# Performance work log

Measured on AMD Instinct MI355X. Metric: run time of the kernel, lower is better.

The kernel has to match this reference:

```python
import jax, jax.numpy as jnp
import numpy as np

NPG = 400          # nodes per graph (CC400 atlas ROIs)
B = 512            # graphs per batch
N = B * NPG        # total nodes
EPG = 6400         # edges per graph (avg degree 16)
E = B * EPG
F_IN = 200         # node feature dim
H = 64             # hidden_channels
C = 2              # num_classes


def _lin(k, fi, fo):
    return jax.random.normal(k, (fi, fo), jnp.float32) / np.sqrt(fi)


def setup_inputs() -> dict:
    key = jax.random.key(0)
    ks = jax.random.split(key, 16)
    # intra-graph edges: local src/dst in [0, NPG) plus per-graph offset
    g = jnp.repeat(jnp.arange(B, dtype=jnp.int32), EPG)
    src = jax.random.randint(ks[0], (E,), 0, NPG, dtype=jnp.int32) + g * NPG
    dst = jax.random.randint(ks[1], (E,), 0, NPG, dtype=jnp.int32) + g * NPG
    edge_index = jnp.stack([src, dst])  # [2, E]
    x = jax.random.normal(ks[2], (N, F_IN), jnp.float32)
    return dict(
        x=x, edge_index=edge_index, npg=NPG,
        # SAGEConv i: out = lin_l(mean_agg) + lin_r(x); lin_l carries the bias
        W1l=_lin(ks[3], F_IN, H), W1r=_lin(ks[4], F_IN, H), b1=jnp.zeros((H,), jnp.float32),
        W2l=_lin(ks[5], H, H), W2r=_lin(ks[6], H, H), b2=jnp.zeros((H,), jnp.float32),
        W3l=_lin(ks[7], H, H), W3r=_lin(ks[8], H, H), b3=jnp.zeros((H,), jnp.float32),
        # SAGPooling score GNN = GraphConv(H, 1): lin_rel(sum_agg) + lin_root(x)
        Wpr=_lin(ks[9], H, 1), bpr=jnp.zeros((1,), jnp.float32), Wpo=_lin(ks[10], H, 1),
        # final classifier
        Wlin=_lin(ks[11], H, C), blin=jnp.zeros((C,), jnp.float32),
    )


def reference(x, edge_index, npg, W1l, W1r, b1, W2l, W2r, b2, W3l, W3r, b3,
              Wpr, bpr, Wpo, Wlin, blin):
    n = x.shape[0]
    src, dst = edge_index[0], edge_index[1]

    deg = jax.ops.segment_sum(jnp.ones((src.shape[0],), x.dtype), dst, num_segments=n)
    inv_deg = 1.0 / jnp.maximum(deg, 1.0)  # [n]

    def sage(h, Wl, Wr, b):
        # mean aggregation over incoming edges, then lin_l(agg)+b + lin_r(h)
        agg = jax.ops.segment_sum(h[src], dst, num_segments=n) * inv_deg[:, None]
        return agg @ Wl + b + h @ Wr

    x1 = jax.nn.relu(sage(x, W1l, W1r, b1))
    x2 = jax.nn.relu(sage(x1, W2l, W2r, b2)) + x1
    x3 = jax.nn.relu(sage(x2, W3l, W3r, b3)) + x2

    # SAGPooling score via GraphConv (add aggregation)
    score = (jax.ops.segment_sum(x3[src], dst, num_segments=n) @ Wpr + bpr
             + x3 @ Wpo)[:, 0]  # [n]

    nb = n // npg            # number of graphs
    k = npg // 2             # ratio = 0.5, uniform graph sizes
    vals, idx = jax.lax.top_k(score.reshape(nb, npg), k)       # [nb, k]
    flat_idx = (jnp.arange(nb, dtype=idx.dtype)[:, None] * npg + idx).reshape(-1)
    xp = x3[flat_idx] * jnp.tanh(vals.reshape(-1))[:, None]    # [nb*k, H]

    pooled = xp.reshape(nb, k, -1).mean(axis=1)                # global_mean_pool
    logits = pooled @ Wlin + blin
    return jax.nn.log_softmax(logits, axis=1)
```

## Files before the change

kernel.cpp:

```cpp
#include <hip/hip_runtime.h>
#include <hip/hip_bf16.h>
#include <math.h>

#define F_IN 200
#define HDIM 64
#define NPG  400
#define EPG  6400
#define KSEL 200

typedef __attribute__((ext_vector_type(4))) float f32x4;
typedef __attribute__((ext_vector_type(8))) short s16x8;
typedef __attribute__((ext_vector_type(4))) unsigned short u16x4;
typedef __attribute__((ext_vector_type(8))) unsigned short u16x8;

__device__ __forceinline__ void gload_lds16(const void* g, void* l) {
    __builtin_amdgcn_global_load_lds(
        (const __attribute__((address_space(1))) void*)g,
        (__attribute__((address_space(3))) void*)l, 16, 0, 0);
}

__device__ __forceinline__ unsigned int bf16_rne(float x) {
    unsigned int b = __float_as_uint(x);
    return (b + 0x7FFFu + ((b >> 16) & 1u)) >> 16;
}
__device__ __forceinline__ float frombf(unsigned short u) {
    return __uint_as_float(((unsigned int)u) << 16);
}

__device__ __forceinline__ void split8(f32x4 v0, f32x4 v1, s16x8& h, s16x8& l) {
    float x[8] = {v0.x, v0.y, v0.z, v0.w, v1.x, v1.y, v1.z, v1.w};
#pragma unroll
    for (int j = 0; j < 8; j++) {
        unsigned int hb = bf16_rne(x[j]);
        float hf = __uint_as_float(hb << 16);
        float r = x[j] - hf;
        unsigned int lb = bf16_rne(r);
        h[j] = (short)hb;
        l[j] = (short)lb;
    }
}

__global__ void pack_wf(const float* __restrict__ Wl, const float* __restrict__ Wr,
                        short* __restrict__ WF, int K, int KC) {
    int idx = blockIdx.x * blockDim.x + threadIdx.x;
    if (idx >= KC * 4096) return;
    int j    = idx & 7;
    int lane = (idx >> 3) & 63;
    int nf   = (idx >> 9) & 7;
    int kc   = idx >> 12;
    int k = kc * 32 + (lane >> 4) * 8 + j;
    int n = nf * 16 + (lane & 15);
    float v = 0.f;
    if (k < K) v = (n < 64) ? Wl[k * 64 + n] : Wr[k * 64 + (n - 64)];
    unsigned int hb = bf16_rne(v);
    float hf = __uint_as_float(hb << 16);
    unsigned int lb = bf16_rne(v - hf);
    WF[(size_t)((kc * 8 + nf) * 2 + 0) * 512 + lane * 8 + j] = (short)hb;
    WF[(size_t)((kc * 8 + nf) * 2 + 1) * 512 + lane * 8 + j] = (short)lb;
}

__global__ void pack_wf4(const float* __restrict__ Wl, const float* __restrict__ Wr,
                         short* __restrict__ WF) {
    int idx = blockIdx.x * blockDim.x + threadIdx.x;
    if (idx >= 4 * 2048) return;
    int j    = idx & 7;
    int lane = (idx >> 3) & 63;
    int nf   = (idx >> 9) & 3;
    int kc   = idx >> 11;
    int k = kc * 32 + (lane >> 4) * 8 + j;
    int n = nf * 16 + (lane & 15);
    float v = (k < 64) ? Wl[k * 64 + n] : Wr[(k - 64) * 64 + n];
    unsigned int hb = bf16_rne(v);
    float hf = __uint_as_float(hb << 16);
    unsigned int lb = bf16_rne(v - hf);
    WF[(size_t)((kc * 4 + nf) * 2 + 0) * 512 + lane * 8 + j] = (short)hb;
    WF[(size_t)((kc * 4 + nf) * 2 + 1) * 512 + lane * 8 + j] = (short)lb;
}

template <int K, int LDX, int KC, int TAIL>
__global__ __launch_bounds__(256) void gemm_lds(const float* __restrict__ X,
                                                const short* __restrict__ WF,
                                                unsigned short* __restrict__ O) {
    __shared__ float Xs[2][128 * 32];
    __shared__ short Ws[2][8 * 2 * 512];
    const int tid  = threadIdx.x;
    const int lane = tid & 63;
    const int wave = tid >> 6;
    const size_t rowbase = (size_t)blockIdx.x * 128;
    const f32x4 zero4 = (f32x4){0.f, 0.f, 0.f, 0.f};

    const int srow_off = wave * 32 + (lane >> 3);
    const int sbyte    = 16 * ((lane & 7) ^ (lane >> 3));

#define DMA_CHUNK(b, kc_) {                                                      \
    _Pragma("unroll")                                                            \
    for (int j = 0; j < 4; j++) {                                                \
        const char* xsrc = (const char*)X +                                      \
            (rowbase + srow_off + j * 8) * (size_t)(LDX * 4) + (kc_) * 128 + sbyte; \
        gload_lds16(xsrc, (char*)&Xs[b][0] + wave * 4096 + j * 1024);            \
        const short* wsrc = WF + (size_t)(kc_) * 8192 + wave * 2048 + j * 512 + lane * 8; \
        gload_lds16(wsrc, (char*)&Ws[b][0] + wave * 4096 + j * 1024);            \
    } }

    f32x4 acc[2][8];
#pragma unroll
    for (int m = 0; m < 2; m++)
#pragma unroll
        for (int nf = 0; nf < 8; nf++) acc[m][nf] = zero4;

    DMA_CHUNK(0, 0);
    __syncthreads();

    for (int kc = 0; kc < KC; kc++) {
        const int b = kc & 1;
        if (kc + 1 < KC) DMA_CHUNK(b ^ 1, kc + 1);

        s16x8 ah[2], al[2];
#pragma unroll
        for (int m = 0; m < 2; m++) {
            const int lr = wave * 32 + m * 16 + (lane & 15);
            const int g0 = (lane >> 4) * 2;
            f32x4 v0 = *(const f32x4*)&Xs[b][lr * 32 + 4 * (g0 ^ (lane & 7))];
            f32x4 v1 = *(const f32x4*)&Xs[b][lr * 32 + 4 * ((g0 + 1) ^ (lane & 7))];
            split8(v0, v1, ah[m], al[m]);
        }
#pragma unroll
        for (int nf = 0; nf < 8; nf++) {
            s16x8 wh = *(const s16x8*)&Ws[b][(nf * 2 + 0) * 512 + lane * 8];
            s16x8 wl = *(const s16x8*)&Ws[b][(nf * 2 + 1) * 512 + lane * 8];
#pragma unroll
            for (int m = 0; m < 2; m++) {
                acc[m][nf] = __builtin_amdgcn_mfma_f32_16x16x32_bf16(ah[m], wh, acc[m][nf], 0, 0, 0);
                acc[m][nf] = __builtin_amdgcn_mfma_f32_16x16x32_bf16(al[m], wh, acc[m][nf], 0, 0, 0);
                acc[m][nf] = __builtin_amdgcn_mfma_f32_16x16x32_bf16(ah[m], wl, acc[m][nf], 0, 0, 0);
            }
        }
        __syncthreads();
    }
#undef DMA_CHUNK

    if constexpr (TAIL > 0) {
        s16x8 ah[2], al[2];
#pragma unroll
        for (int m = 0; m < 2; m++) {
            const size_t row = rowbase + wave * 32 + m * 16 + (lane & 15);
            const int k0 = KC * 32 + (lane >> 4) * 8;
            f32x4 v0 = (k0 + 4 <= K) ? *(const f32x4*)&X[row * (size_t)LDX + k0] : zero4;
            f32x4 v1 = (k0 + 8 <= K) ? *(const f32x4*)&X[row * (size_t)LDX + k0 + 4] : zero4;
            split8(v0, v1, ah[m], al[m]);
        }
#pragma unroll
        for (int nf = 0; nf < 8; nf++) {
            s16x8 wh = *(const s16x8*)&WF[(size_t)((KC * 8 + nf) * 2 + 0) * 512 + lane * 8];
            s16x8 wl = *(const s16x8*)&WF[(size_t)((KC * 8 + nf) * 2 + 1) * 512 + lane * 8];
#pragma unroll
            for (int m = 0; m < 2; m++) {
                acc[m][nf] = __builtin_amdgcn_mfma_f32_16x16x32_bf16(ah[m], wh, acc[m][nf], 0, 0, 0);
                acc[m][nf] = __builtin_amdgcn_mfma_f32_16x16x32_bf16(al[m], wh, acc[m][nf], 0, 0, 0);
                acc[m][nf] = __builtin_amdgcn_mfma_f32_16x16x32_bf16(ah[m], wl, acc[m][nf], 0, 0, 0);
            }
        }
    }

    float* cs0 = &Xs[0][wave * 1024];
    float* cs1 = &Xs[1][wave * 1024];
#pragma unroll
    for (int m = 0; m < 2; m++) {
        const int scol = lane & 15;
        const int srow = (lane >> 4) * 4;
#pragma unroll
        for (int nf = 0; nf < 8; nf++)
#pragma unroll
            for (int r = 0; r < 4; r++) {
                int cr = srow + r;
                float* p = (cr < 8) ? cs0 + cr * 128 : cs1 + (cr - 8) * 128;
                p[nf * 16 + scol] = acc[m][nf][r];
            }
#pragma unroll
        for (int ps = 0; ps < 8; ps++) {
            int row = ps * 2 + (lane >> 5);
            int col = (lane & 31) * 4;
            const float* p = (row < 8) ? cs0 + row * 128 : cs1 + (row - 8) * 128;
            f32x4 v = *(const f32x4*)&p[col];
            u16x4 o;
#pragma unroll
            for (int q = 0; q < 4; q++) o[q] = (unsigned short)bf16_rne(v[q]);
            *(u16x4*)&O[(rowbase + wave * 32 + m * 16 + row) * 128 + col] = o;
        }
    }
}

__global__ __launch_bounds__(256) void combine_ss(
    const float* __restrict__ M, const float* __restrict__ H,
    const short* __restrict__ WF, const float* __restrict__ bias,
    const float* __restrict__ resid, float* __restrict__ P)
{
    __shared__ float Xs[4][64 * 32];
    __shared__ short Ws[4][4096];
    const int tid  = threadIdx.x;
    const int lane = tid & 63;
    const int wave = tid >> 6;
    const size_t rowbase = (size_t)blockIdx.x * 64;

    f32x4 rr[4], bb;
    {
        const int col = (lane & 15) * 4;
        bb = *(const f32x4*)&bias[col];
#pragma unroll
        for (int i = 0; i < 4; i++) {
            int row = i * 4 + (lane >> 4);
            size_t grow = rowbase + wave * 16 + row;
            rr[i] = *(const f32x4*)&resid[grow * 64 + col];
        }
    }

#pragma unroll
    for (int c = 0; c < 4; c++) {
        const float* srcbuf = (c < 2) ? M : H;
#pragma unroll
        for (int i = 0; i < 2; i++) {
            int rr2 = i * 8 + (lane >> 3);
            int jj = (lane & 7) ^ (rr2 & 7);
            const char* src = (const char*)(srcbuf + (rowbase + wave * 16 + rr2) * 64)
                              + (c & 1) * 128 + jj * 16;
            gload_lds16(src, (char*)&Xs[c][0] + wave * 2048 + i * 1024 + lane * 16);
        }
#pragma unroll
        for (int t = 0; t < 2; t++) {
            int idx = t * 256 + tid;
            const short* wsrc = WF + (size_t)c * 4096 + idx * 8;
            gload_lds16(wsrc, (char*)&Ws[c][0] + idx * 16);
        }
    }
    __syncthreads();

    f32x4 acc[4];
#pragma unroll
    for (int nf = 0; nf < 4; nf++) acc[nf] = (f32x4){0.f, 0.f, 0.f, 0.f};

    const int r = lane & 15;
    const int j0 = (lane >> 4) * 2;
#pragma unroll
    for (int kc = 0; kc < 4; kc++) {
        const float* abase = &Xs[kc][wave * 512 + r * 32];
        f32x4 v0 = *(const f32x4*)&abase[((j0    ) ^ (r & 7)) * 4];
        f32x4 v1 = *(const f32x4*)&abase[((j0 + 1) ^ (r & 7)) * 4];
        s16x8 ah, al;
        split8(v0, v1, ah, al);
#pragma unroll
        for (int nf = 0; nf < 4; nf++) {
            s16x8 wh = *(const s16x8*)&Ws[kc][(nf * 2 + 0) * 512 + lane * 8];
            s16x8 wl = *(const s16x8*)&Ws[kc][(nf * 2 + 1) * 512 + lane * 8];
            acc[nf] = __builtin_amdgcn_mfma_f32_16x16x32_bf16(ah, wh, acc[nf], 0, 0, 0);
            acc[nf] = __builtin_amdgcn_mfma_f32_16x16x32_bf16(al, wh, acc[nf], 0, 0, 0);
            acc[nf] = __builtin_amdgcn_mfma_f32_16x16x32_bf16(ah, wl, acc[nf], 0, 0, 0);
        }
    }

    {
        float* cs0 = &Xs[0][wave * 512];
        float* cs1 = &Xs[1][wave * 512];
        const int scol = lane & 15;
        const int srow = (lane >> 4) * 4;
#pragma unroll
        for (int nf = 0; nf < 4; nf++)
#pragma unroll
            for (int ri = 0; ri < 4; ri++) {
                int cr = srow + ri;
                float* p = (cr < 8) ? cs0 + cr * 64 : cs1 + (cr - 8) * 64;
                p[nf * 16 + scol] = acc[nf][ri];
            }
#pragma unroll
        for (int i = 0; i < 4; i++) {
            int row = i * 4 + (lane >> 4);
            int col = (lane & 15) * 4;
            const float* p = (row < 8) ? cs0 + row * 64 : cs1 + (row - 8) * 64;
            f32x4 v = *(const f32x4*)&p[col];
            size_t grow = rowbase + wave * 16 + row;
            f32x4 o;
#pragma unroll
            for (int q = 0; q < 4; q++) o[q] = fmaxf(v[q] + bb[q], 0.f) + rr[i][q];
            *(f32x4*)&P[grow * 64 + col] = o;
        }
    }
}

__global__ __launch_bounds__(256) void csr_build(
    const int* __restrict__ esrc, const int* __restrict__ edst,
    int* __restrict__ csr_src, int* __restrict__ rowptr,
    int* __restrict__ degs, float* __restrict__ invdeg)
{
    __shared__ int cnt[NPG];
    __shared__ int off[NPG];
    __shared__ int cur[NPG];
    const int g = blockIdx.x, tid = threadIdx.x;
    const int ebase = g * EPG, nodebase = g * NPG;
    for (int i = tid; i < NPG; i += 256) cnt[i] = 0;
    __syncthreads();
    for (int e = tid; e < EPG; e += 256)
        atomicAdd(&cnt[edst[ebase + e] - nodebase], 1);
    __syncthreads();
    if (tid == 0) {
        int run = 0;
        for (int i = 0; i < NPG; i++) { off[i] = run; run += cnt[i]; }
    }
    __syncthreads();
    for (int i = tid; i < NPG; i += 256) {
        cur[i] = off[i];
        rowptr[nodebase + i] = off[i];
        degs[nodebase + i] = cnt[i];
        invdeg[nodebase + i] = 1.f / fmaxf((float)cnt[i], 1.f);
    }
    __syncthreads();
    for (int e = tid; e < EPG; e += 256) {
        int ld = edst[ebase + e] - nodebase;
        int p = atomicAdd(&cur[ld], 1);
        csr_src[ebase + p] = esrc[ebase + e] - nodebase;
    }
}

__global__ __launch_bounds__(1024) void agg_lds(
    const unsigned short* __restrict__ A,
    const int* __restrict__ csr_src, const int* __restrict__ rowptr,
    const int* __restrict__ degs, const float* __restrict__ invdeg,
    const float* __restrict__ bias,
    float* __restrict__ Xout)
{
    __shared__ float y[NPG * 64];
    __shared__ int   csr_l[EPG];
    const int g = blockIdx.x, tid = threadIdx.x;
    const int ebase = g * EPG, nodebase = g * NPG;

    for (int idx = tid; idx < NPG * 8; idx += 1024) {
        int node = idx >> 3, c8 = (idx & 7) * 8;
        u16x8 v = *(const u16x8*)&A[(size_t)(nodebase + node) * 128 + c8];
#pragma unroll
        for (int q = 0; q < 8; q++) y[node * 64 + c8 + q] = frombf(v[q]);
    }
    for (int e = tid; e < EPG; e += 1024) csr_l[e] = csr_src[ebase + e];
    __syncthreads();

    const int wave = tid >> 6, lane = tid & 63;
    for (int node = wave; node < NPG; node += 16) {
        const int start = rowptr[nodebase + node];
        const int dg = degs[nodebase + node];
        float acc = 0.f;
        int j = 0;
        for (; j + 4 <= dg; j += 4) {
            int s0 = csr_l[start + j];
            int s1 = csr_l[start + j + 1];
            int s2 = csr_l[start + j + 2];
            int s3 = csr_l[start + j + 3];
            acc += y[s0 * 64 + lane] + y[s1 * 64 + lane]
                 + y[s2 * 64 + lane] + y[s3 * 64 + lane];
        }
        for (; j < dg; j++) acc += y[csr_l[start + j] * 64 + lane];

        float z = frombf(A[(size_t)(nodebase + node) * 128 + 64 + lane]);
        float v = acc * invdeg[nodebase + node] + bias[lane] + z;
        Xout[(size_t)(nodebase + node) * 64 + lane] = fmaxf(v, 0.f);
    }
}

__global__ __launch_bounds__(1024) void agg_in(
    const float* __restrict__ H,
    const int* __restrict__ csr_src, const int* __restrict__ rowptr,
    const int* __restrict__ degs, const float* __restrict__ invdeg,
    float* __restrict__ M)
{
    __shared__ float y[NPG * 64];
    __shared__ int   csr_l[EPG];
    const int g = blockIdx.x, tid = threadIdx.x;
    const int ebase = g * EPG, nodebase = g * NPG;

    for (int idx = tid; idx < NPG * 16; idx += 1024) {
        int node = idx >> 4, c4 = (idx & 15) * 4;
        *(float4*)&y[node * 64 + c4] =
            *(const float4*)&H[(size_t)(nodebase + node) * 64 + c4];
    }
    for (int e = tid; e < EPG; e += 1024) csr_l[e] = csr_src[ebase + e];
    __syncthreads();

    const int wave = tid >> 6, lane = tid & 63;
    for (int node = wave; node < NPG; node += 16) {
        const int start = rowptr[nodebase + node];
        const int dg = degs[nodebase + node];
        float acc = 0.f;
        int j = 0;
        for (; j + 4 <= dg; j += 4) {
            int s0 = csr_l[start + j];
            int s1 = csr_l[start + j + 1];
            int s2 = csr_l[start + j + 2];
            int s3 = csr_l[start + j + 3];
            acc += y[s0 * 64 + lane] + y[s1 * 64 + lane]
                 + y[s2 * 64 + lane] + y[s3 * 64 + lane];
        }
        for (; j < dg; j++) acc += y[csr_l[start + j] * 64 + lane];

        M[(size_t)(nodebase + node) * 64 + lane] = acc * invdeg[nodebase + node];
    }
}

__global__ __launch_bounds__(1024) void score_pool3(
    const float* __restrict__ X3,
    const int* __restrict__ esrc, const int* __restrict__ edst,
    const float* __restrict__ Wpr, const float* __restrict__ bpr,
    const float* __restrict__ Wpo,
    const float* __restrict__ Wlin, const float* __restrict__ blin,
    float* __restrict__ out)
{
    __shared__ float y[NPG * 64];
    __shared__ float t0s[NPG], ss[NPG], wsel[NPG];
    __shared__ float wprs[64], wpos[64];
    __shared__ float pp[16 * 64];
    __shared__ float pooled[64];
    __shared__ float lgs[2];
    const int g = blockIdx.x, tid = threadIdx.x;
    const int nodebase = g * NPG, ebase = g * EPG;

    if (tid < 64) { wprs[tid] = Wpr[tid]; wpos[tid] = Wpo[tid]; }
    for (int idx = tid; idx < NPG * 16; idx += 1024) {
        int node = idx >> 4, c4 = (idx & 15) * 4;
        *(float4*)&y[node * 64 + c4] =
            *(const float4*)&X3[(size_t)(nodebase + node) * 64 + c4];
    }
    __syncthreads();

    if (tid < NPG) {
        float a0 = 0.f, a1 = 0.f;
        const float* yr = &y[tid * 64];
#pragma unroll
        for (int i = 0; i < 64; i++) {
            int d = (tid + i) & 63;
            float v = yr[d];
            a0 += v * wprs[d];
            a1 += v * wpos[d];
        }
        t0s[tid] = a0;
        ss[tid] = bpr[0] + a1;
    }
    __syncthreads();
    for (int e = tid; e < EPG; e += 1024) {
        int ls = esrc[ebase + e] - nodebase;
        int ld = edst[ebase + e] - nodebase;
        atomicAdd(&ss[ld], t0s[ls]);
    }
    __syncthreads();
    if (tid < NPG) {
        float si = ss[tid];
        int cnt = 0;
        for (int j = 0; j < NPG; j++) {
            float sj = ss[j];
            cnt += (sj > si) || (sj == si && j < tid);
        }
        wsel[tid] = (cnt < KSEL) ? tanhf(si) * (1.f / KSEL) : 0.f;
    }
    __syncthreads();
    {
        const int d = tid & 63, part = tid >> 6;
        float a = 0.f;
        for (int i = part * 25; i < part * 25 + 25; i++)
            a += wsel[i] * y[i * 64 + d];
        pp[part * 64 + d] = a;
    }
    __syncthreads();
    if (tid < 64) {
        float s = 0.f;
#pragma unroll
        for (int i = 0; i < 16; i++) s += pp[i * 64 + tid];
        pooled[tid] = s;
    }
    __syncthreads();
    if (tid < 2) {
        float l = blin[tid];
        for (int d = 0; d < 64; d++) l += pooled[d] * Wlin[d * 2 + tid];
        lgs[tid] = l;
    }
    __syncthreads();
    if (tid < 2) {
        float m = fmaxf(lgs[0], lgs[1]);
        float lse = m + logf(expf(lgs[0] - m) + expf(lgs[1] - m));
        out[g * 2 + tid] = lgs[tid] - lse;
    }
}

extern "C" void kernel_launch(void* const* d_in, const int* in_sizes, int n_in,
                              void* d_out, int out_size, void* d_ws, size_t ws_size,
                              hipStream_t stream) {
    const float* x    = (const float*)d_in[0];
    const int*   eidx = (const int*)d_in[1];
    const float* W1l  = (const float*)d_in[3];
    const float* W1r  = (const float*)d_in[4];
    const float* b1   = (const float*)d_in[5];
    const float* W2l  = (const float*)d_in[6];
    const float* W2r  = (const float*)d_in[7];
    const float* b2   = (const float*)d_in[8];
    const float* W3l  = (const float*)d_in[9];
    const float* W3r  = (const float*)d_in[10];
    const float* b3   = (const float*)d_in[11];
    const float* Wpr  = (const float*)d_in[12];
    const float* bpr  = (const float*)d_in[13];
    const float* Wpo  = (const float*)d_in[14];
    const float* Wlin = (const float*)d_in[15];
    const float* blin = (const float*)d_in[16];

    const int N = in_sizes[0] / F_IN;
    const int E = in_sizes[1] / 2;
    const int B = N / NPG;
    const int* esrc = eidx;
    const int* edst = eidx + E;

    float* ws = (float*)d_ws;
    unsigned short* A = (unsigned short*)ws;
    float* P0     = ws + (size_t)N * 64;
    float* P1     = P0 + (size_t)N * 64;
    float* Mb     = P1 + (size_t)N * 64;
    float* invdeg = Mb + (size_t)N * 64;
    short* WF1    = (short*)(invdeg + N);
    short* WFc2   = WF1 + 57344;
    short* WFc3   = WFc2 + 16384;
    int*   csr    = (int*)(WFc3 + 16384);
    int*   rowptr = csr + E;
    int*   degs   = rowptr + N;

    pack_wf<<<(7 * 4096 + 255) / 256, 256, 0, stream>>>(W1l, W1r, WF1, 200, 7);
    pack_wf4<<<(4 * 2048 + 255) / 256, 256, 0, stream>>>(W2l, W2r, WFc2);
    pack_wf4<<<(4 * 2048 + 255) / 256, 256, 0, stream>>>(W3l, W3r, WFc3);

    csr_build<<<B, 256, 0, stream>>>(esrc, edst, csr, rowptr, degs, invdeg);

    gemm_lds<200, 200, 6, 8><<<N / 128, 256, 0, stream>>>(x, WF1, A);
    agg_lds<<<B, 1024, 0, stream>>>(A, csr, rowptr, degs, invdeg, b1, P0);

    agg_in<<<B, 1024, 0, stream>>>(P0, csr, rowptr, degs, invdeg, Mb);
    combine_ss<<<N / 64, 256, 0, stream>>>(Mb, P0, WFc2, b2, P0, P1);

    agg_in<<<B, 1024, 0, stream>>>(P1, csr, rowptr, degs, invdeg, Mb);
    combine_ss<<<N / 64, 256, 0, stream>>>(Mb, P1, WFc3, b3, P1, P0);

    score_pool3<<<B, 1024, 0, stream>>>(P0, esrc, edst,
                                        Wpr, bpr, Wpo, Wlin, blin,
                                        (float*)d_out);
}
```

Measured before the change: 419.0 us.

## Store intermediate activations in bf16 and drop split-precision MFMA in combine

Hidden activations (P0, P1) and mean-aggregated features (Mb) now live in bf16 instead of fp32. Every producer and consumer kernel is updated: agg_lds, agg_in, combine and score_pool3. Global memory traffic for these intermediates is halved. The combine GEMM loads bf16 A fragments straight from global memory, skipping the LDS staging and the hi/lo split, so the MFMA count drops from three to two per step. The cost is lower precision in the activations and the residual path, which may hurt accuracy.

```diff
diff --git a/kernel.cpp b/kernel.cpp
--- a/kernel.cpp
+++ b/kernel.cpp
@@ -190,13 +190,13 @@
     }
 }
 
-__global__ __launch_bounds__(256) void combine_ss(
-    const float* __restrict__ M, const float* __restrict__ H,
+__global__ __launch_bounds__(256) void combine_bf(
+    const unsigned short* __restrict__ Mb, const unsigned short* __restrict__ Hb,
     const short* __restrict__ WF, const float* __restrict__ bias,
-    const float* __restrict__ resid, float* __restrict__ P)
+    unsigned short* __restrict__ P)
 {
-    __shared__ float Xs[4][64 * 32];
     __shared__ short Ws[4][4096];
+    __shared__ float Cs[2][4 * 512];
     const int tid  = threadIdx.x;
     const int lane = tid & 63;
     const int wave = tid >> 6;
@@ -210,56 +210,49 @@
         for (int i = 0; i < 4; i++) {
             int row = i * 4 + (lane >> 4);
             size_t grow = rowbase + wave * 16 + row;
-            rr[i] = *(const f32x4*)&resid[grow * 64 + col];
-        }
-    }
-
-#pragma unroll
-    for (int c = 0; c < 4; c++) {
-        const float* srcbuf = (c < 2) ? M : H;
-#pragma unroll
-        for (int i = 0; i < 2; i++) {
-            int rr2 = i * 8 + (lane >> 3);
-            int jj = (lane & 7) ^ (rr2 & 7);
-            const char* src = (const char*)(srcbuf + (rowbase + wave * 16 + rr2) * 64)
-                              + (c & 1) * 128 + jj * 16;
-            gload_lds16(src, (char*)&Xs[c][0] + wave * 2048 + i * 1024 + lane * 16);
-        }
+            u16x4 h4 = *(const u16x4*)&Hb[grow * 64 + col];
+#pragma unroll
+            for (int q = 0; q < 4; q++) rr[i][q] = frombf(h4[q]);
+        }
+    }
+
+#pragma unroll
+    for (int c = 0; c < 4; c++)
 #pragma unroll
         for (int t = 0; t < 2; t++) {
             int idx = t * 256 + tid;
             const short* wsrc = WF + (size_t)c * 4096 + idx * 8;
             gload_lds16(wsrc, (char*)&Ws[c][0] + idx * 16);
         }
-    }
+
+    const size_t arow = rowbase + wave * 16 + (lane & 15);
+    const int kq = (lane >> 4) * 8;
+    s16x8 ah[4];
+    ah[0] = *(const s16x8*)&Mb[arow * 64 + kq];
+    ah[1] = *(const s16x8*)&Mb[arow * 64 + 32 + kq];
+    ah[2] = *(const s16x8*)&Hb[arow * 64 + kq];
+    ah[3] = *(const s16x8*)&Hb[arow * 64 + 32 + kq];
+
     __syncthreads();
 
     f32x4 acc[4];
 #pragma unroll
     for (int nf = 0; nf < 4; nf++) acc[nf] = (f32x4){0.f, 0.f, 0.f, 0.f};
 
-    const int r = lane & 15;
-    const int j0 = (lane >> 4) * 2;
 #pragma unroll
     for (int kc = 0; kc < 4; kc++) {
-        const float* abase = &Xs[kc][wave * 512 + r * 32];
-        f32x4 v0 = *(const f32x4*)&abase[((j0    ) ^ (r & 7)) * 4];
-        f32x4 v1 = *(const f32x4*)&abase[((j0 + 1) ^ (r & 7)) * 4];
-        s16x8 ah, al;
-        split8(v0, v1, ah, al);
 #pragma unroll
         for (int nf = 0; nf < 4; nf++) {
             s16x8 wh = *(const s16x8*)&Ws[kc][(nf * 2 + 0) * 512 + lane * 8];
             s16x8 wl = *(const s16x8*)&Ws[kc][(nf * 2 + 1) * 512 + lane * 8];
-            acc[nf] = __builtin_amdgcn_mfma_f32_16x16x32_bf16(ah, wh, acc[nf], 0, 0, 0);
-            acc[nf] = __builtin_amdgcn_mfma_f32_16x16x32_bf16(al, wh, acc[nf], 0, 0, 0);
-            acc[nf] = __builtin_amdgcn_mfma_f32_16x16x32_bf16(ah, wl, acc[nf], 0, 0, 0);
+            acc[nf] = __builtin_amdgcn_mfma_f32_16x16x32_bf16(ah[kc], wh, acc[nf], 0, 0, 0);
+            acc[nf] = __builtin_amdgcn_mfma_f32_16x16x32_bf16(ah[kc], wl, acc[nf], 0, 0, 0);
         }
     }
 
     {
-        float* cs0 = &Xs[0][wave * 512];
-        float* cs1 = &Xs[1][wave * 512];
+        float* cs0 = &Cs[0][wave * 512];
+        float* cs1 = &Cs[1][wave * 512];
         const int scol = lane & 15;
         const int srow = (lane >> 4) * 4;
 #pragma unroll
@@ -277,10 +270,11 @@
             const float* p = (row < 8) ? cs0 + row * 64 : cs1 + (row - 8) * 64;
             f32x4 v = *(const f32x4*)&p[col];
             size_t grow = rowbase + wave * 16 + row;
-            f32x4 o;
-#pragma unroll
-            for (int q = 0; q < 4; q++) o[q] = fmaxf(v[q] + bb[q], 0.f) + rr[i][q];
-            *(f32x4*)&P[grow * 64 + col] = o;
+            u16x4 o;
+#pragma unroll
+            for (int q = 0; q < 4; q++)
+                o[q] = (unsigned short)bf16_rne(fmaxf(v[q] + bb[q], 0.f) + rr[i][q]);
+            *(u16x4*)&P[grow * 64 + col] = o;
         }
     }
 }
@@ -324,7 +318,7 @@
     const int* __restrict__ csr_src, const int* __restrict__ rowptr,
     const int* __restrict__ degs, const float* __restrict__ invdeg,
     const float* __restrict__ bias,
-    float* __restrict__ Xout)
+    unsigned short* __restrict__ Xout)
 {
     __shared__ float y[NPG * 64];
     __shared__ int   csr_l[EPG];
@@ -358,25 +352,27 @@
 
         float z = frombf(A[(size_t)(nodebase + node) * 128 + 64 + lane]);
         float v = acc * invdeg[nodebase + node] + bias[lane] + z;
-        Xout[(size_t)(nodebase + node) * 64 + lane] = fmaxf(v, 0.f);
+        Xout[(size_t)(nodebase + node) * 64 + lane] =
+            (unsigned short)bf16_rne(fmaxf(v, 0.f));
     }
 }
 
 __global__ __launch_bounds__(1024) void agg_in(
-    const float* __restrict__ H,
+    const unsigned short* __restrict__ H,
     const int* __restrict__ csr_src, const int* __restrict__ rowptr,
     const int* __restrict__ degs, const float* __restrict__ invdeg,
-    float* __restrict__ M)
+    unsigned short* __restrict__ M)
 {
     __shared__ float y[NPG * 64];
     __shared__ int   csr_l[EPG];
     const int g = blockIdx.x, tid = threadIdx.x;
     const int ebase = g * EPG, nodebase = g * NPG;
 
-    for (int idx = tid; idx < NPG * 16; idx += 1024) {
-        int node = idx >> 4, c4 = (idx & 15) * 4;
-        *(float4*)&y[node * 64 + c4] =
-            *(const float4*)&H[(size_t)(nodebase + node) * 64 + c4];
+    for (int idx = tid; idx < NPG * 8; idx += 1024) {
+        int node = idx >> 3, c8 = (idx & 7) * 8;
+        u16x8 v = *(const u16x8*)&H[(size_t)(nodebase + node) * 64 + c8];
+#pragma unroll
+        for (int q = 0; q < 8; q++) y[node * 64 + c8 + q] = frombf(v[q]);
     }
     for (int e = tid; e < EPG; e += 1024) csr_l[e] = csr_src[ebase + e];
     __syncthreads();
@@ -397,12 +393,13 @@
         }
         for (; j < dg; j++) acc += y[csr_l[start + j] * 64 + lane];
 
-        M[(size_t)(nodebase + node) * 64 + lane] = acc * invdeg[nodebase + node];
+        M[(size_t)(nodebase + node) * 64 + lane] =
+            (unsigned short)bf16_rne(acc * invdeg[nodebase + node]);
     }
 }
 
 __global__ __launch_bounds__(1024) void score_pool3(
-    const float* __restrict__ X3,
+    const unsigned short* __restrict__ X3,
     const int* __restrict__ esrc, const int* __restrict__ edst,
     const float* __restrict__ Wpr, const float* __restrict__ bpr,
     const float* __restrict__ Wpo,
@@ -419,10 +416,11 @@
     const int nodebase = g * NPG, ebase = g * EPG;
 
     if (tid < 64) { wprs[tid] = Wpr[tid]; wpos[tid] = Wpo[tid]; }
-    for (int idx = tid; idx < NPG * 16; idx += 1024) {
-        int node = idx >> 4, c4 = (idx & 15) * 4;
-        *(float4*)&y[node * 64 + c4] =
-            *(const float4*)&X3[(size_t)(nodebase + node) * 64 + c4];
+    for (int idx = tid; idx < NPG * 8; idx += 1024) {
+        int node = idx >> 3, c8 = (idx & 7) * 8;
+        u16x8 v = *(const u16x8*)&X3[(size_t)(nodebase + node) * 64 + c8];
+#pragma unroll
+        for (int q = 0; q < 8; q++) y[node * 64 + c8 + q] = frombf(v[q]);
     }
     __syncthreads();
 
@@ -511,11 +509,11 @@
     const int* edst = eidx + E;
 
     float* ws = (float*)d_ws;
-    unsigned short* A = (unsigned short*)ws;
-    float* P0     = ws + (size_t)N * 64;
-    float* P1     = P0 + (size_t)N * 64;
-    float* Mb     = P1 + (size_t)N * 64;
-    float* invdeg = Mb + (size_t)N * 64;
+    unsigned short* A   = (unsigned short*)ws;
+    unsigned short* P0  = (unsigned short*)(ws + (size_t)N * 64);
+    unsigned short* P1  = P0 + (size_t)N * 64;
+    unsigned short* Mb  = P1 + (size_t)N * 64;
+    float* invdeg = (float*)(Mb + (size_t)N * 64);
     short* WF1    = (short*)(invdeg + N);
     short* WFc2   = WF1 + 57344;
     short* WFc3   = WFc2 + 16384;
@@ -533,10 +531,10 @@
     agg_lds<<<B, 1024, 0, stream>>>(A, csr, rowptr, degs, invdeg, b1, P0);
 
     agg_in<<<B, 1024, 0, stream>>>(P0, csr, rowptr, degs, invdeg, Mb);
-    combine_ss<<<N / 64, 256, 0, stream>>>(Mb, P0, WFc2, b2, P0, P1);
+    combine_bf<<<N / 64, 256, 0, stream>>>(Mb, P0, WFc2, b2, P1);
 
     agg_in<<<B, 1024, 0, stream>>>(P1, csr, rowptr, degs, invdeg, Mb);
-    combine_ss<<<N / 64, 256, 0, stream>>>(Mb, P1, WFc3, b3, P1, P0);
+    combine_bf<<<N / 64, 256, 0, stream>>>(Mb, P1, WFc3, b3, P0);
 
     score_pool3<<<B, 1024, 0, stream>>>(P0, esrc, edst,
                                         Wpr, bpr, Wpo, Wlin, blin,
```

New measurement: 384.9 us (median of 2 runs). 1.09x faster.
